# Kernel tuning notes

Measured on AMD Instinct MI355X. Metric: run time of the kernel, lower is better.

## Reference

```python
import jax, jax.numpy as jnp
import numpy as np

LN_EPS = 1e-5

def _ln(x, g, b):
    m = x.mean(-1, keepdims=True)
    v = ((x - m) ** 2).mean(-1, keepdims=True)
    return (x - m) / jnp.sqrt(v + LN_EPS) * g + b

def _mlp(x, W1, b1, g, beta, W2, b2):
    # Linear -> LayerNorm -> ReLU -> Linear
    h = jax.nn.relu(_ln(x @ W1 + b1, g, beta))
    return h @ W2 + b2

def setup_inputs() -> dict:
    key = jax.random.key(0)
    N, E, C_in, C_out, H = 50000, 800000, 64, 64, 64
    ks = jax.random.split(key, 16)
    def rn(k, shape, fan_in):
        return jax.random.normal(k, shape, jnp.float32) * (fan_in ** -0.5)
    return dict(
        x=jax.random.normal(ks[0], (N, C_in), jnp.float32),
        pos=jax.random.normal(ks[1], (N, 3), jnp.float32),
        edge_index=jax.random.randint(ks[2], (2, E), 0, N, jnp.int32),
        W_in=rn(ks[3], (C_in, C_in), C_in), b_in=jnp.zeros((C_in,), jnp.float32),
        W_lin=rn(ks[4], (C_in, C_out), C_in),
        W_src=rn(ks[5], (C_in, C_out), C_in),
        W_dst=rn(ks[6], (C_in, C_out), C_in),
        pos_W1=rn(ks[7], (3, H), 3), pos_b1=jnp.zeros((H,), jnp.float32),
        pos_g=jnp.ones((H,), jnp.float32), pos_beta=jnp.zeros((H,), jnp.float32),
        pos_W2=rn(ks[8], (H, C_out), H), pos_b2=jnp.zeros((C_out,), jnp.float32),
        att_W1=rn(ks[9], (C_out, H), C_out), att_b1=jnp.zeros((H,), jnp.float32),
        att_g=jnp.ones((H,), jnp.float32), att_beta=jnp.zeros((H,), jnp.float32),
        att_W2=rn(ks[10], (H, C_out), H), att_b2=jnp.zeros((C_out,), jnp.float32),
        W_out=rn(ks[11], (C_out, C_out), C_out), b_out=jnp.zeros((C_out,), jnp.float32),
    )

def reference(x, pos, edge_index, W_in, b_in, W_lin, W_src, W_dst,
              pos_W1, pos_b1, pos_g, pos_beta, pos_W2, pos_b2,
              att_W1, att_b1, att_g, att_beta, att_W2, att_b2,
              W_out, b_out):
    N = x.shape[0]
    # lin_in + relu
    x = jax.nn.relu(x @ W_in + b_in)
    # PointTransformerConv with add_self_loops=True (PyG default)
    loops = jnp.arange(N, dtype=edge_index.dtype)
    src = jnp.concatenate([edge_index[0], loops])  # j (neighbors)
    dst = jnp.concatenate([edge_index[1], loops])  # i (centers)
    a_src = x @ W_src           # [N, C_out]
    a_dst = x @ W_dst           # [N, C_out]
    v = x @ W_lin               # [N, C_out]
    # per-edge positional encoding delta = pos_nn(pos_i - pos_j)
    delta = _mlp(pos[dst] - pos[src], pos_W1, pos_b1, pos_g, pos_beta, pos_W2, pos_b2)  # [E, C_out]
    alpha = _mlp(a_dst[dst] - a_src[src] + delta, att_W1, att_b1, att_g, att_beta, att_W2, att_b2)
    # per-destination, per-channel softmax over variable-size neighborhoods
    amax = jax.ops.segment_max(alpha, dst, num_segments=N)
    e = jnp.exp(alpha - amax[dst])
    denom = jax.ops.segment_sum(e, dst, num_segments=N)
    w = e / jnp.clip(denom[dst], 1e-16)
    # weighted scatter-sum of (value_j + delta)
    out = jax.ops.segment_sum(w * (v[src] + delta), dst, num_segments=N)  # [N, C_out]
    # lin_out + relu
    return jax.nn.relu(out @ W_out + b_out)
```

## Files before the change

### kernel.cpp

```cpp
#include <hip/hip_runtime.h>
#include <hip/hip_bf16.h>


typedef __bf16 bf16x8 __attribute__((ext_vector_type(8)));
typedef short  s16x8  __attribute__((ext_vector_type(8)));
typedef float  f32x4  __attribute__((ext_vector_type(4)));

#define SWZ(b) ((b) ^ ((((b) >> 7) & 7) << 4))

__device__ __forceinline__ unsigned short f2b(float f) {
  union { __hip_bfloat16 h; unsigned short u; } c;
  c.h = __float2bfloat16(f);
  return c.u;
}
__device__ __forceinline__ unsigned int pack2(float a, float b) {
  return (unsigned int)f2b(a) | ((unsigned int)f2b(b) << 16);
}
__device__ __forceinline__ void unpack2(unsigned int u, float& a, float& b) {
  union { unsigned int x; float f; } t0, t1;
  t0.x = u << 16; t1.x = u & 0xffff0000u;
  a = t0.f; b = t1.f;
}
__device__ __forceinline__ void lds_fence() {
  asm volatile("s_waitcnt lgkmcnt(0)" ::: "memory");
  __builtin_amdgcn_sched_barrier(0);
}
__device__ __forceinline__ f32x4 psel(bool p, f32x4 a) {
  f32x4 z = {0.f, 0.f, 0.f, 0.f};
  return p ? a : z;
}
template <int D>
__device__ __forceinline__ f32x4 shup4(f32x4 v) {
  f32x4 r;
  #pragma unroll
  for (int c = 0; c < 4; c++) r[c] = __shfl_up(v[c], D);
  return r;
}

__device__ __forceinline__ int sigp(int p) { return 4 * (p & 15) + (p >> 4); }

__device__ __forceinline__ void stage_wt(const float* __restrict__ W, char* dst, int tid) {
  for (int idx = tid; idx < 2048; idx += 256) {
    int c  = idx >> 5;
    int k2 = (idx & 31) << 1;
    *(unsigned int*)(dst + SWZ(c * 128 + k2 * 2)) = pack2(W[k2 * 64 + c], W[(k2 + 1) * 64 + c]);
  }
}
__device__ __forceinline__ void stage_wt_sig(const float* __restrict__ W, char* dst, int tid) {
  for (int idx = tid; idx < 2048; idx += 256) {
    int q  = idx >> 5;
    int p2 = (idx & 31) << 1;
    int co = sigp(q);
    *(unsigned int*)(dst + SWZ(q * 128 + p2 * 2)) =
        pack2(W[sigp(p2) * 64 + co], W[sigp(p2 + 1) * 64 + co]);
  }
}

__device__ __forceinline__ void gemm16(const char* actb, const char* wb,
                                       int g, int m, f32x4 acc[4]) {
  #pragma unroll
  for (int kk = 0; kk < 2; kk++) {
    s16x8 af = *(const s16x8*)(actb + SWZ(m * 128 + g * 16 + kk * 64));
    #pragma unroll
    for (int t = 0; t < 4; t++) {
      s16x8 bf = *(const s16x8*)(wb + SWZ((t * 16 + m) * 128 + g * 16 + kk * 64));
      acc[t] = __builtin_amdgcn_mfma_f32_16x16x32_bf16(
          __builtin_bit_cast(bf16x8, af), __builtin_bit_cast(bf16x8, bf), acc[t], 0, 0, 0);
    }
  }
}

__global__ __launch_bounds__(256, 3) void node_mfma_kernel(
    const float* __restrict__ x,
    const float* __restrict__ W_in, const float* __restrict__ b_in,
    const float* __restrict__ W_lin, const float* __restrict__ W_src, const float* __restrict__ W_dst,
    unsigned short* __restrict__ a_srcB, unsigned short* __restrict__ a_dstB,
    unsigned short* __restrict__ vB, int N)
{
  __shared__ __align__(16) char sWinT[8192], sWsT[8192], sWdT[8192], sWlT[8192], sX[8192];
  __shared__ __align__(16) float sB[64];
  int tid = threadIdx.x;
  stage_wt(W_in,  sWinT, tid);
  stage_wt(W_src, sWsT,  tid);
  stage_wt(W_dst, sWdT,  tid);
  stage_wt(W_lin, sWlT,  tid);
  if (tid < 64) sB[tid] = b_in[tid];

  const int lane = tid & 63, wv = tid >> 6;
  const int g = lane >> 4, m = lane & 15;
  const int ew = wv << 4;
  const int srow = tid >> 2, sc0 = (tid & 3) << 4;
  const int ntile = (N + 63) >> 6;

  for (int tile = blockIdx.x; tile < ntile; tile += gridDim.x) {
    const int rbase = tile << 6;
    __syncthreads();
    {
      int gr = rbase + srow; if (gr >= N) gr = N - 1;
      const float4* src = (const float4*)&x[(size_t)gr * 64 + sc0];
      #pragma unroll
      for (int q = 0; q < 4; q++) {
        float4 f = src[q];
        int byte = srow * 128 + sc0 * 2 + q * 8;
        *(unsigned int*)(sX + SWZ(byte))     = pack2(f.x, f.y);
        *(unsigned int*)(sX + SWZ(byte + 4)) = pack2(f.z, f.w);
      }
    }
    __syncthreads();

    f32x4 a0[4] = {};
    gemm16(sX + ew * 128, sWinT, g, m, a0);
    float x1[4][4];
    #pragma unroll
    for (int t = 0; t < 4; t++)
      #pragma unroll
      for (int r = 0; r < 4; r++) x1[t][r] = fmaxf(a0[t][r] + sB[t * 16 + m], 0.f);
    __syncthreads();
    #pragma unroll
    for (int t = 0; t < 4; t++)
      #pragma unroll
      for (int r = 0; r < 4; r++)
        *(unsigned short*)(sX + SWZ((ew + 4 * g + r) * 128 + (t * 16 + m) * 2)) = f2b(x1[t][r]);
    __syncthreads();

    f32x4 as[4] = {}, ad[4] = {}, al[4] = {};
    gemm16(sX + ew * 128, sWsT, g, m, as);
    gemm16(sX + ew * 128, sWdT, g, m, ad);
    gemm16(sX + ew * 128, sWlT, g, m, al);
    #pragma unroll
    for (int t = 0; t < 4; t++)
      #pragma unroll
      for (int r = 0; r < 4; r++) {
        int gr = rbase + ew + 4 * g + r;
        if (gr < N) {
          size_t o = (size_t)gr * 64 + t * 16 + m;
          a_srcB[o] = f2b(as[t][r]); a_dstB[o] = f2b(ad[t][r]); vB[o] = f2b(al[t][r]);
        }
      }
  }
}

__global__ void hist_kernel(const int* __restrict__ ei, int* __restrict__ deg, int E, int Etot) {
  int stride = gridDim.x * blockDim.x;
  for (int e = blockIdx.x * blockDim.x + threadIdx.x; e < Etot; e += stride) {
    int d = (e < E) ? ei[E + e] : (e - E);
    atomicAdd(&deg[d], 1);
  }
}

__global__ __launch_bounds__(256) void scanA_kernel(const int* __restrict__ deg, int* __restrict__ chunkSum, int N) {
  __shared__ int s[256];
  int i = blockIdx.x * 256 + threadIdx.x;
  s[threadIdx.x] = (i < N) ? deg[i] : 0;
  __syncthreads();
  for (int off = 128; off > 0; off >>= 1) {
    if (threadIdx.x < off) s[threadIdx.x] += s[threadIdx.x + off];
    __syncthreads();
  }
  if (threadIdx.x == 0) chunkSum[blockIdx.x] = s[0];
}

__global__ __launch_bounds__(256) void scanB_kernel(const int* __restrict__ chunkSum, int* __restrict__ chunkPre, int nchunk) {
  __shared__ int s[256];
  int t = threadIdx.x;
  int v = (t < nchunk) ? chunkSum[t] : 0;
  s[t] = v; __syncthreads();
  for (int off = 1; off < 256; off <<= 1) {
    int x = (t >= off) ? s[t - off] : 0;
    __syncthreads();
    s[t] += x;
    __syncthreads();
  }
  if (t < nchunk) chunkPre[t] = s[t] - v;
}

__global__ __launch_bounds__(256) void scanC_kernel(const int* __restrict__ deg, const int* __restrict__ chunkPre,
                                                    int* __restrict__ cursor, int N) {
  __shared__ int s[256];
  int t = threadIdx.x;
  int i = blockIdx.x * 256 + t;
  int v = (i < N) ? deg[i] : 0;
  s[t] = v; __syncthreads();
  for (int off = 1; off < 256; off <<= 1) {
    int x = (t >= off) ? s[t - off] : 0;
    __syncthreads();
    s[t] += x;
    __syncthreads();
  }
  if (i < N) cursor[i] = chunkPre[blockIdx.x] + s[t] - v;
}

__global__ void scatter_kernel(const int* __restrict__ ei, int* __restrict__ cursor,
                               const float* __restrict__ pos,
                               int* __restrict__ srcS, int* __restrict__ dstS,
                               float4* __restrict__ pd4,
                               int E, int Etot) {
  int stride = gridDim.x * blockDim.x;
  for (int e = blockIdx.x * blockDim.x + threadIdx.x; e < Etot; e += stride) {
    int s, d;
    if (e < E) { s = ei[e]; d = ei[E + e]; }
    else       { s = e - E; d = s; }
    int p = atomicAdd(&cursor[d], 1);
    srcS[p] = s; dstS[p] = d;
    float4 q;
    q.x = pos[d * 3 + 0] - pos[s * 3 + 0];
    q.y = pos[d * 3 + 1] - pos[s * 3 + 1];
    q.z = pos[d * 3 + 2] - pos[s * 3 + 2];
    q.w = 0.f;
    pd4[p] = q;
  }
}

struct Meta { int md[4]; int ms[4]; f32x4 pd[4]; };
struct Gath { uint2 ad[4]; uint2 as[4]; uint2 vv[4]; };

__device__ __forceinline__ Meta load_meta(const int* __restrict__ dstS, const int* __restrict__ srcS,
                                          const float4* __restrict__ pd4, int ebase, int g) {
  Meta M;
  int4 a = *(const int4*)&dstS[ebase + 4 * g];
  int4 b = *(const int4*)&srcS[ebase + 4 * g];
  M.md[0] = a.x; M.md[1] = a.y; M.md[2] = a.z; M.md[3] = a.w;
  M.ms[0] = b.x; M.ms[1] = b.y; M.ms[2] = b.z; M.ms[3] = b.w;
  #pragma unroll
  for (int r = 0; r < 4; r++) {
    float4 p = pd4[ebase + 4 * g + r];
    M.pd[r][0] = p.x; M.pd[r][1] = p.y; M.pd[r][2] = p.z; M.pd[r][3] = 0.f;
  }
  return M;
}
__device__ __forceinline__ Gath load_gath(const Meta& M,
                                          const unsigned short* __restrict__ aD,
                                          const unsigned short* __restrict__ aS,
                                          const unsigned short* __restrict__ vB, int m) {
  Gath G;
  #pragma unroll
  for (int r = 0; r < 4; r++) {
    int dm = M.md[r] < 0 ? 0 : M.md[r];
    G.ad[r] = *(const uint2*)&aD[(size_t)dm * 64 + 4 * m];
    G.as[r] = *(const uint2*)&aS[(size_t)M.ms[r] * 64 + 4 * m];
    G.vv[r] = *(const uint2*)&vB[(size_t)M.ms[r] * 64 + 4 * m];
  }
  return G;
}

__global__ __launch_bounds__(256, 3) void edge_kernel(
    const int* __restrict__ srcS, const int* __restrict__ dstS, const float4* __restrict__ pd4,
    const unsigned short* __restrict__ a_srcB, const unsigned short* __restrict__ a_dstB,
    const unsigned short* __restrict__ vBg,
    const float* __restrict__ pos_W1, const float* __restrict__ pos_b1,
    const float* __restrict__ pos_gg, const float* __restrict__ pos_beta,
    const float* __restrict__ pos_W2, const float* __restrict__ pos_b2,
    const float* __restrict__ att_W1, const float* __restrict__ att_b1,
    const float* __restrict__ att_gg, const float* __restrict__ att_beta,
    const float* __restrict__ att_W2, const float* __restrict__ att_b2,
    float* __restrict__ numer, float* __restrict__ denom,
    int G, int gpw)
{
  __shared__ __align__(16) char sW2t[8192], sA1t[8192], sA2t[8192];
  __shared__ __align__(16) char sAct[4][2048];
  __shared__ __align__(16) float sPW1[192];
  __shared__ __align__(16) float sPB1[64], sPG[64], sPBeta[64], sPB2[64];
  __shared__ __align__(16) float sAB1[64], sAG[64], sABeta[64], sAB2[64];

  int tid = threadIdx.x;
  stage_wt_sig(pos_W2, sW2t, tid);
  stage_wt_sig(att_W1, sA1t, tid);
  stage_wt_sig(att_W2, sA2t, tid);
  for (int i = tid; i < 192; i += 256) sPW1[i] = pos_W1[i];
  if (tid < 64) {
    sPB1[tid] = pos_b1[tid]; sPG[tid] = pos_gg[tid]; sPBeta[tid] = pos_beta[tid]; sPB2[tid] = pos_b2[tid];
    sAB1[tid] = att_b1[tid]; sAG[tid] = att_gg[tid]; sABeta[tid] = att_beta[tid]; sAB2[tid] = att_b2[tid];
  }
  __syncthreads();

  const int lane = tid & 63, wv = tid >> 6;
  const int g = lane >> 4, m = lane & 15;
  char* myAct = sAct[wv];

  const int w  = blockIdx.x * 4 + wv;
  const int g0 = w * gpw;
  int g1 = g0 + gpw; if (g1 > G) g1 = G;
  if (g0 >= g1) return;

  const f32x4 pw0 = *(const f32x4*)&sPW1[4 * m];
  const f32x4 pw1 = *(const f32x4*)&sPW1[64 + 4 * m];
  const f32x4 pw2 = *(const f32x4*)&sPW1[128 + 4 * m];
  const f32x4 pb1 = *(const f32x4*)&sPB1[4 * m];
  const f32x4 pgv = *(const f32x4*)&sPG[4 * m];
  const f32x4 pbv = *(const f32x4*)&sPBeta[4 * m];
  const f32x4 pb2 = *(const f32x4*)&sPB2[4 * m];
  const f32x4 ab1 = *(const f32x4*)&sAB1[4 * m];
  const f32x4 agv = *(const f32x4*)&sAG[4 * m];
  const f32x4 abv = *(const f32x4*)&sABeta[4 * m];
  const f32x4 ab2 = *(const f32x4*)&sAB2[4 * m];

  Meta Mc = load_meta(dstS, srcS, pd4, g0 << 4, g);
  Gath Gc = load_gath(Mc, a_dstB, a_srcB, vBg, m);

  for (int grp = g0; grp < g1; ++grp) {
    const int gnext = (grp + 1 < g1) ? grp + 1 : grp;
    Meta Mn = load_meta(dstS, srcS, pd4, gnext << 4, g);

    f32x4 hA[4];
    #pragma unroll
    for (int r = 0; r < 4; r++) {
      f32x4 h = pb1 + pw0 * Mc.pd[r][0] + pw1 * Mc.pd[r][1] + pw2 * Mc.pd[r][2];
      float s = h[0] + h[1] + h[2] + h[3];
      s += __shfl_xor(s, 1); s += __shfl_xor(s, 2); s += __shfl_xor(s, 4); s += __shfl_xor(s, 8);
      float mean = s * (1.f / 64.f);
      f32x4 dv = h - mean;
      float q = dv[0]*dv[0] + dv[1]*dv[1] + dv[2]*dv[2] + dv[3]*dv[3];
      q += __shfl_xor(q, 1); q += __shfl_xor(q, 2); q += __shfl_xor(q, 4); q += __shfl_xor(q, 8);
      float rs = rsqrtf(q * (1.f / 64.f) + 1e-5f);
      f32x4 o = dv * rs * pgv + pbv;
      #pragma unroll
      for (int c = 0; c < 4; c++) o[c] = fmaxf(o[c], 0.f);
      hA[r] = o;
    }
    #pragma unroll
    for (int r = 0; r < 4; r++)
      #pragma unroll
      for (int t = 0; t < 4; t++)
        *(unsigned short*)(myAct + SWZ((4 * g + r) * 128 + 32 * t + 2 * m)) = f2b(hA[r][t]);
    lds_fence();

    f32x4 dacc[4] = {};
    gemm16(myAct, sW2t, g, m, dacc);
    f32x4 del[4];
    #pragma unroll
    for (int t = 0; t < 4; t++) del[t] = dacc[t] + pb2[t];

    #pragma unroll
    for (int r = 0; r < 4; r++) {
      float da[4], sa[4];
      unpack2(Gc.ad[r].x, da[0], da[1]); unpack2(Gc.ad[r].y, da[2], da[3]);
      unpack2(Gc.as[r].x, sa[0], sa[1]); unpack2(Gc.as[r].y, sa[2], sa[3]);
      #pragma unroll
      for (int t = 0; t < 4; t++) {
        float av = da[t] - sa[t] + del[t][r];
        *(unsigned short*)(myAct + SWZ((4 * g + r) * 128 + 32 * t + 2 * m)) = f2b(av);
      }
    }
    lds_fence();

    f32x4 acc2[4] = {};
    gemm16(myAct, sA1t, g, m, acc2);
    f32x4 h2[4];
    #pragma unroll
    for (int t = 0; t < 4; t++) h2[t] = acc2[t] + ab1[t];
    #pragma unroll
    for (int r = 0; r < 4; r++) {
      float s = h2[0][r] + h2[1][r] + h2[2][r] + h2[3][r];
      s += __shfl_xor(s, 1); s += __shfl_xor(s, 2); s += __shfl_xor(s, 4); s += __shfl_xor(s, 8);
      float mean = s * (1.f / 64.f);
      float q = 0.f;
      #pragma unroll
      for (int t = 0; t < 4; t++) { float dd = h2[t][r] - mean; q = fmaf(dd, dd, q); }
      q += __shfl_xor(q, 1); q += __shfl_xor(q, 2); q += __shfl_xor(q, 4); q += __shfl_xor(q, 8);
      float rs = rsqrtf(q * (1.f / 64.f) + 1e-5f);
      #pragma unroll
      for (int t = 0; t < 4; t++)
        h2[t][r] = fmaxf(fmaf((h2[t][r] - mean) * rs, agv[t], abv[t]), 0.f);
    }
    #pragma unroll
    for (int r = 0; r < 4; r++)
      #pragma unroll
      for (int t = 0; t < 4; t++)
        *(unsigned short*)(myAct + SWZ((4 * g + r) * 128 + 32 * t + 2 * m)) = f2b(h2[t][r]);
    lds_fence();

    f32x4 acc3[4] = {};
    gemm16(myAct, sA2t, g, m, acc3);

    Gath Gn = load_gath(Mn, a_dstB, a_srcB, vBg, m);

    f32x4 nV[4], dV[4];
    #pragma unroll
    for (int r = 0; r < 4; r++) {
      float vf[4];
      unpack2(Gc.vv[r].x, vf[0], vf[1]); unpack2(Gc.vv[r].y, vf[2], vf[3]);
      bool val = Mc.md[r] >= 0;
      #pragma unroll
      for (int t = 0; t < 4; t++) {
        float e = __expf(acc3[t][r] + ab2[t]);
        e = val ? e : 0.f;
        nV[r][t] = e * (vf[t] + del[t][r]);
        dV[r][t] = e;
      }
    }

    {
      int d3 = Mc.md[3];
      bool s2 = (Mc.md[2] == d3);
      bool s1 = s2 && (Mc.md[1] == d3);
      bool s0 = s1 && (Mc.md[0] == d3);
      f32x4 PN = nV[3] + psel(s2, nV[2]) + psel(s1, nV[1]) + psel(s0, nV[0]);
      f32x4 PD = dV[3] + psel(s2, dV[2]) + psel(s1, dV[1]) + psel(s0, dV[0]);

      int dPrev3 = __shfl_up(d3, 16);
      int dNext0 = __shfl_down(Mc.md[0], 16);
      bool ok1 = (g > 0) && (Mc.md[0] == dPrev3);
      int okf = (ok1 && s0) ? 1 : 0;
      int okf1 = __shfl_up(okf, 16);
      int okf2 = __shfl_up(okf, 32);
      bool ok2 = ok1 && (okf1 != 0);
      bool ok3 = ok2 && (okf2 != 0);
      f32x4 sh16N = shup4<16>(PN), sh32N = shup4<32>(PN), sh48N = shup4<48>(PN);
      f32x4 sh16D = shup4<16>(PD), sh32D = shup4<32>(PD), sh48D = shup4<48>(PD);
      f32x4 CN = psel(ok1, sh16N) + psel(ok2, sh32N) + psel(ok3, sh48N);
      f32x4 CD = psel(ok1, sh16D) + psel(ok2, sh32D) + psel(ok3, sh48D);

      int dn[4] = { Mc.md[1], Mc.md[2], Mc.md[3], (g == 3) ? (int)0x80000000 : dNext0 };

      f32x4 aN = CN, aD = CD;
      #pragma unroll
      for (int r = 0; r < 4; r++) {
        aN += nV[r]; aD += dV[r];
        if (Mc.md[r] != dn[r]) {
          if (Mc.md[r] >= 0) {
            float* np = &numer[(size_t)Mc.md[r] * 64 + 4 * m];
            float* dp = &denom[(size_t)Mc.md[r] * 64 + 4 * m];
            #pragma unroll
            for (int t = 0; t < 4; t++) { atomicAdd(np + t, aN[t]); atomicAdd(dp + t, aD[t]); }
          }
          f32x4 z = {0.f, 0.f, 0.f, 0.f};
          aN = z; aD = z;
        }
      }
    }

    Mc = Mn; Gc = Gn;
  }
}

__global__ __launch_bounds__(256) void out_mfma_kernel(
    const float* __restrict__ numer, const float* __restrict__ denom,
    const float* __restrict__ W_out, const float* __restrict__ b_out,
    float* __restrict__ out, int N)
{
  __shared__ __align__(16) char sWoT[8192], sX[8192];
  __shared__ float sB[64];
  int tid = threadIdx.x;
  stage_wt(W_out, sWoT, tid);
  if (tid < 64) sB[tid] = b_out[tid];

  const int lane = tid & 63, wv = tid >> 6;
  const int g = lane >> 4, m = lane & 15;
  const int ew = wv << 4;
  const int srow = tid >> 2, sc0 = (tid & 3) << 4;
  const int ntile = (N + 63) >> 6;

  for (int tile = blockIdx.x; tile < ntile; tile += gridDim.x) {
    const int rbase = tile << 6;
    __syncthreads();
    {
      int gr = rbase + srow; if (gr >= N) gr = N - 1;
      const float4* nsrc = (const float4*)&numer[(size_t)gr * 64 + sc0];
      const float4* dsrc = (const float4*)&denom[(size_t)gr * 64 + sc0];
      #pragma unroll
      for (int q = 0; q < 4; q++) {
        float4 fn = nsrc[q], fd = dsrc[q];
        float m0 = fn.x / fmaxf(fd.x, 1e-16f);
        float m1 = fn.y / fmaxf(fd.y, 1e-16f);
        float m2 = fn.z / fmaxf(fd.z, 1e-16f);
        float m3 = fn.w / fmaxf(fd.w, 1e-16f);
        int byte = srow * 128 + sc0 * 2 + q * 8;
        *(unsigned int*)(sX + SWZ(byte))     = pack2(m0, m1);
        *(unsigned int*)(sX + SWZ(byte + 4)) = pack2(m2, m3);
      }
    }
    __syncthreads();
    f32x4 acc[4] = {};
    gemm16(sX + ew * 128, sWoT, g, m, acc);
    #pragma unroll
    for (int t = 0; t < 4; t++)
      #pragma unroll
      for (int r = 0; r < 4; r++) {
        int gr = rbase + ew + 4 * g + r;
        if (gr < N) out[(size_t)gr * 64 + t * 16 + m] = fmaxf(acc[t][r] + sB[t * 16 + m], 0.f);
      }
  }
}

extern "C" void kernel_launch(void* const* d_in, const int* in_sizes, int n_in,
                              void* d_out, int out_size, void* d_ws, size_t ws_size,
                              hipStream_t stream) {
  (void)n_in; (void)out_size; (void)ws_size;
  const float* x        = (const float*)d_in[0];
  const float* pos      = (const float*)d_in[1];
  const int*   ei       = (const int*)  d_in[2];
  const float* W_in     = (const float*)d_in[3];
  const float* b_in     = (const float*)d_in[4];
  const float* W_lin    = (const float*)d_in[5];
  const float* W_src    = (const float*)d_in[6];
  const float* W_dst    = (const float*)d_in[7];
  const float* pos_W1   = (const float*)d_in[8];
  const float* pos_b1   = (const float*)d_in[9];
  const float* pos_g    = (const float*)d_in[10];
  const float* pos_beta = (const float*)d_in[11];
  const float* pos_W2   = (const float*)d_in[12];
  const float* pos_b2   = (const float*)d_in[13];
  const float* att_W1   = (const float*)d_in[14];
  const float* att_b1   = (const float*)d_in[15];
  const float* att_g    = (const float*)d_in[16];
  const float* att_beta = (const float*)d_in[17];
  const float* att_W2   = (const float*)d_in[18];
  const float* att_b2   = (const float*)d_in[19];
  const float* W_out    = (const float*)d_in[20];
  const float* b_out    = (const float*)d_in[21];

  const int N    = in_sizes[0] / 64;
  const int E    = in_sizes[2] / 2;
  const int Etot = E + N;
  const int Epad = (Etot + 15) & ~15;
  const size_t N64 = (size_t)N * 64;

  float* numer = (float*)d_ws;
  float* denom = numer + N64;
  unsigned short* aSb = (unsigned short*)(denom + N64);
  unsigned short* aDb = aSb + N64;
  unsigned short* vBb = aDb + N64;
  float4* pd4 = (float4*)(vBb + N64);
  int* srcS     = (int*)(pd4 + Epad);
  int* dstS     = srcS + Epad;
  int* deg      = dstS + Epad;
  int* cursor   = deg + N;
  int* chunkSum = cursor + N;
  int* chunkPre = chunkSum + 256;

  const int nchunk = (N + 255) / 256;

  hipMemsetAsync(deg, 0, (size_t)N * sizeof(int), stream);
  hipMemsetAsync(numer, 0, 2 * N64 * sizeof(float), stream);
  if (Epad > Etot) {
    hipMemsetAsync(dstS + Etot, 0xFF, (size_t)(Epad - Etot) * sizeof(int), stream);
    hipMemsetAsync(srcS + Etot, 0, (size_t)(Epad - Etot) * sizeof(int), stream);
    hipMemsetAsync(pd4 + Etot, 0, (size_t)(Epad - Etot) * sizeof(float4), stream);
  }

  hist_kernel<<<1024, 256, 0, stream>>>(ei, deg, E, Etot);
  scanA_kernel<<<nchunk, 256, 0, stream>>>(deg, chunkSum, N);
  scanB_kernel<<<1, 256, 0, stream>>>(chunkSum, chunkPre, nchunk);
  scanC_kernel<<<nchunk, 256, 0, stream>>>(deg, chunkPre, cursor, N);
  scatter_kernel<<<1024, 256, 0, stream>>>(ei, cursor, pos, srcS, dstS, pd4, E, Etot);

  const int ntileN = (N + 63) / 64;
  const int nblkN  = ntileN < 768 ? ntileN : 768;
  node_mfma_kernel<<<nblkN, 256, 0, stream>>>(x, W_in, b_in, W_lin, W_src, W_dst,
                                              aSb, aDb, vBb, N);

  const int G   = Epad / 16;
  const int NB  = 768;
  const int gpw = (G + NB * 4 - 1) / (NB * 4);
  edge_kernel<<<NB, 256, 0, stream>>>(srcS, dstS, pd4, aSb, aDb, vBb,
      pos_W1, pos_b1, pos_g, pos_beta, pos_W2, pos_b2,
      att_W1, att_b1, att_g, att_beta, att_W2, att_b2,
      numer, denom, G, gpw);

  out_mfma_kernel<<<nblkN, 256, 0, stream>>>(numer, denom, W_out, b_out, (float*)d_out, N);
}
```

Before: 431.1 us.

## Use DPP row-rotate reductions, raise occupancy, prefetch gathers earlier, set MFMA priority

Replaces the shfl_xor butterfly reductions inside the LayerNorm steps with DPP row_ror adds within 16 lanes, which avoids LDS-routed shuffles. Raises the edge kernel's launch bound to 4 blocks per CU and the grid from 768 to 1024 blocks. Moves the next group's gather loads before the second GEMM so they have more time to arrive, and raises wave priority around the MFMA GEMMs. The added occupancy and the longer-lived prefetch registers both push on the register budget, so spills or lower ILP are possible.

```diff
diff --git a/kernel.cpp b/kernel.cpp
--- a/kernel.cpp
+++ b/kernel.cpp
@@ -35,6 +35,16 @@
   #pragma unroll
   for (int c = 0; c < 4; c++) r[c] = __shfl_up(v[c], D);
   return r;
+}
+
+template <int N>
+__device__ __forceinline__ float ror16(float x) {
+  return __builtin_bit_cast(float,
+      __builtin_amdgcn_update_dpp(0, __builtin_bit_cast(int, x), 0x120 + N, 0xF, 0xF, false));
+}
+__device__ __forceinline__ float rsum16(float s) {
+  s += ror16<1>(s); s += ror16<2>(s); s += ror16<4>(s); s += ror16<8>(s);
+  return s;
 }
 
 __device__ __forceinline__ int sigp(int p) { return 4 * (p & 15) + (p >> 4); }
@@ -243,7 +253,7 @@
   return G;
 }
 
-__global__ __launch_bounds__(256, 3) void edge_kernel(
+__global__ __launch_bounds__(256, 4) void edge_kernel(
     const int* __restrict__ srcS, const int* __restrict__ dstS, const float4* __restrict__ pd4,
     const unsigned short* __restrict__ a_srcB, const unsigned short* __restrict__ a_dstB,
     const unsigned short* __restrict__ vBg,
@@ -305,12 +315,10 @@
     #pragma unroll
     for (int r = 0; r < 4; r++) {
       f32x4 h = pb1 + pw0 * Mc.pd[r][0] + pw1 * Mc.pd[r][1] + pw2 * Mc.pd[r][2];
-      float s = h[0] + h[1] + h[2] + h[3];
-      s += __shfl_xor(s, 1); s += __shfl_xor(s, 2); s += __shfl_xor(s, 4); s += __shfl_xor(s, 8);
+      float s = rsum16(h[0] + h[1] + h[2] + h[3]);
       float mean = s * (1.f / 64.f);
       f32x4 dv = h - mean;
-      float q = dv[0]*dv[0] + dv[1]*dv[1] + dv[2]*dv[2] + dv[3]*dv[3];
-      q += __shfl_xor(q, 1); q += __shfl_xor(q, 2); q += __shfl_xor(q, 4); q += __shfl_xor(q, 8);
+      float q = rsum16(dv[0]*dv[0] + dv[1]*dv[1] + dv[2]*dv[2] + dv[3]*dv[3]);
       float rs = rsqrtf(q * (1.f / 64.f) + 1e-5f);
       f32x4 o = dv * rs * pgv + pbv;
       #pragma unroll
@@ -325,7 +333,9 @@
     lds_fence();
 
     f32x4 dacc[4] = {};
+    __builtin_amdgcn_s_setprio(1);
     gemm16(myAct, sW2t, g, m, dacc);
+    __builtin_amdgcn_s_setprio(0);
     f32x4 del[4];
     #pragma unroll
     for (int t = 0; t < 4; t++) del[t] = dacc[t] + pb2[t];
@@ -343,20 +353,23 @@
     }
     lds_fence();
 
+    Gath Gn = load_gath(Mn, a_dstB, a_srcB, vBg, m);
+
     f32x4 acc2[4] = {};
+    __builtin_amdgcn_s_setprio(1);
     gemm16(myAct, sA1t, g, m, acc2);
+    __builtin_amdgcn_s_setprio(0);
     f32x4 h2[4];
     #pragma unroll
     for (int t = 0; t < 4; t++) h2[t] = acc2[t] + ab1[t];
     #pragma unroll
     for (int r = 0; r < 4; r++) {
-      float s = h2[0][r] + h2[1][r] + h2[2][r] + h2[3][r];
-      s += __shfl_xor(s, 1); s += __shfl_xor(s, 2); s += __shfl_xor(s, 4); s += __shfl_xor(s, 8);
+      float s = rsum16(h2[0][r] + h2[1][r] + h2[2][r] + h2[3][r]);
       float mean = s * (1.f / 64.f);
-      float q = 0.f;
-      #pragma unroll
-      for (int t = 0; t < 4; t++) { float dd = h2[t][r] - mean; q = fmaf(dd, dd, q); }
-      q += __shfl_xor(q, 1); q += __shfl_xor(q, 2); q += __shfl_xor(q, 4); q += __shfl_xor(q, 8);
+      float q0 = 0.f;
+      #pragma unroll
+      for (int t = 0; t < 4; t++) { float dd = h2[t][r] - mean; q0 = fmaf(dd, dd, q0); }
+      float q = rsum16(q0);
       float rs = rsqrtf(q * (1.f / 64.f) + 1e-5f);
       #pragma unroll
       for (int t = 0; t < 4; t++)
@@ -370,9 +383,9 @@
     lds_fence();
 
     f32x4 acc3[4] = {};
+    __builtin_amdgcn_s_setprio(1);
     gemm16(myAct, sA2t, g, m, acc3);
-
-    Gath Gn = load_gath(Mn, a_dstB, a_srcB, vBg, m);
+    __builtin_amdgcn_s_setprio(0);
 
     f32x4 nV[4], dV[4];
     #pragma unroll
@@ -550,7 +563,7 @@
                                               aSb, aDb, vBb, N);
 
   const int G   = Epad / 16;
-  const int NB  = 768;
+  const int NB  = 1024;
   const int gpw = (G + NB * 4 - 1) / (NB * 4);
   edge_kernel<<<NB, 256, 0, stream>>>(srcS, dstS, pd4, aSb, aDb, vBb,
       pos_W1, pos_b1, pos_g, pos_beta, pos_W2, pos_b2,
```

Result: slower. 555.3 us (+28.8%).
